# Kernel tuning notes

Measured on AMD Instinct MI355X. Metric: run time of the kernel, lower is better.

The kernel has to match this reference:

```python
import jax, jax.numpy as jnp
import numpy as np

N_HEAD = 16
HEAD_DIM = 64
ROPE_BASE = 10000.0


def _rope(t):
    # t: [B, H, C, D]; rotate-half RoPE, offset 0
    B, H, C, D = t.shape
    inv_freq = 1.0 / (ROPE_BASE ** (jnp.arange(0, D, 2, dtype=jnp.float32) / D))  # [D/2]
    ang = jnp.arange(C, dtype=jnp.float32)[:, None] * inv_freq[None, :]           # [C, D/2]
    cos = jnp.concatenate([jnp.cos(ang), jnp.cos(ang)], axis=-1)                  # [C, D]
    sin = jnp.concatenate([jnp.sin(ang), jnp.sin(ang)], axis=-1)                  # [C, D]
    t1, t2 = jnp.split(t, 2, axis=-1)
    rot = jnp.concatenate([-t2, t1], axis=-1)
    return t * cos.astype(t.dtype) + rot * sin.astype(t.dtype)


def setup_inputs() -> dict:
    key = jax.random.key(0)
    ks = jax.random.split(key, 5)
    E = 1024
    B, C = 2, 2048
    s = 1.0 / np.sqrt(E)
    return {
        "x": jax.random.normal(ks[0], (B, C, E), dtype=jnp.float32),
        "Wq": jax.random.normal(ks[1], (E, E), dtype=jnp.float32) * s,
        "Wk": jax.random.normal(ks[2], (E, E), dtype=jnp.float32) * s,
        "Wv": jax.random.normal(ks[3], (E, E), dtype=jnp.float32) * s,
        "Wo": jax.random.normal(ks[4], (E, E), dtype=jnp.float32) * s,
    }


def reference(x, Wq, Wk, Wv, Wo):
    B, C, E = x.shape
    H, D = N_HEAD, HEAD_DIM
    # nn.Linear(bias=False): y = x @ W.T
    Q = (x @ Wq.T).reshape(B, C, H, D).transpose(0, 2, 1, 3)  # [B,H,C,D]
    K = (x @ Wk.T).reshape(B, C, H, D).transpose(0, 2, 1, 3)
    V = (x @ Wv.T).reshape(B, C, H, D).transpose(0, 2, 1, 3)
    Q = _rope(Q)
    K = _rope(K)
    scores = jnp.einsum("bhqd,bhkd->bhqk", Q, K) / jnp.sqrt(jnp.float32(D))
    causal = jnp.tril(jnp.ones((C, C), dtype=bool))
    scores = jnp.where(causal, scores, jnp.float32(-jnp.inf))
    weights = jax.nn.softmax(scores, axis=-1)
    hidden = jnp.einsum("bhqk,bhkd->bhqd", weights, V)
    hidden = hidden.transpose(0, 2, 1, 3).reshape(B, C, H * D)
    return hidden @ Wo.T
```

## Files before the change

### kernel.cpp

```cpp
#include <hip/hip_runtime.h>
#include <hip/hip_bf16.h>

typedef __attribute__((ext_vector_type(8))) short bf16x8;
typedef __attribute__((ext_vector_type(4))) float f32x4;
typedef unsigned short u16;
typedef unsigned int u32;


__device__ __forceinline__ u16 f2bf(float f) {
  __hip_bfloat16 h = __float2bfloat16(f);
  return *reinterpret_cast<u16*>(&h);
}

__device__ __forceinline__ void async16(const void* g, void* l) {
  __builtin_amdgcn_global_load_lds((const __attribute__((address_space(1))) u32*)g,
                                   (__attribute__((address_space(3))) u32*)l, 16, 0, 0);
}


__global__ void cast_bf16(const float4* __restrict__ src, ushort4* __restrict__ dst, int n4) {
  int stride = gridDim.x * blockDim.x;
  for (int i = blockIdx.x * blockDim.x + threadIdx.x; i < n4; i += stride) {
    float4 v = src[i];
    ushort4 o;
    o.x = f2bf(v.x); o.y = f2bf(v.y); o.z = f2bf(v.z); o.w = f2bf(v.w);
    dst[i] = o;
  }
}

__global__ void cast_w4(const float4* __restrict__ w0, const float4* __restrict__ w1,
                        const float4* __restrict__ w2, const float4* __restrict__ w3,
                        ushort4* __restrict__ o0, ushort4* __restrict__ o1,
                        ushort4* __restrict__ o2, ushort4* __restrict__ o3, int n4) {
  const float4* src = (blockIdx.y == 0) ? w0 : (blockIdx.y == 1) ? w1 : (blockIdx.y == 2) ? w2 : w3;
  ushort4* dst = (blockIdx.y == 0) ? o0 : (blockIdx.y == 1) ? o1 : (blockIdx.y == 2) ? o2 : o3;
  int stride = gridDim.x * blockDim.x;
  for (int i = blockIdx.x * blockDim.x + threadIdx.x; i < n4; i += stride) {
    float4 v = src[i];
    ushort4 o;
    o.x = f2bf(v.x); o.y = f2bf(v.y); o.z = f2bf(v.z); o.w = f2bf(v.w);
    dst[i] = o;
  }
}


__global__ void rope_table(float* __restrict__ tcos, float* __restrict__ tsin) {
  int idx = blockIdx.x * blockDim.x + threadIdx.x;
  if (idx >= 2048 * 32) return;
  int c = idx >> 5, j = idx & 31;
  float inv = powf(10000.f, -(float)j * (1.f / 32.f));
  float ang = (float)c * inv;
  tcos[idx] = cosf(ang);
  tsin[idx] = sinf(ang);
}


__launch_bounds__(256)
__global__ void qkv_gemm(const u16* __restrict__ xb, const u16* __restrict__ Wqb,
                         const u16* __restrict__ Wkb, const u16* __restrict__ Wvb,
                         const float* __restrict__ tcos, const float* __restrict__ tsin,
                         u16* __restrict__ Qr, u16* __restrict__ Kr, u16* __restrict__ Vt) {
  const int z = blockIdx.z;
  const u16* W = (z == 0) ? Wqb : (z == 1) ? Wkb : Wvb;
  u16* dst = (z == 0) ? Qr : (z == 1) ? Kr : Vt;
  const int m0 = blockIdx.y * 128, n0 = blockIdx.x * 128;
  const int tid = threadIdx.x, w = tid >> 6, lane = tid & 63, g = lane >> 4, cl = lane & 15;
  const int wr = w >> 1, wc = w & 1;
  __shared__ u16 As[128][32], Bs[128][32];
  f32x4 acc[4][4] = {};
  for (int k0 = 0; k0 < 1024; k0 += 32) {
#pragma unroll
    for (int ch = 0; ch < 2; ++ch) {
      int t = tid + ch * 256;
      int row = t >> 2, col = (t & 3) * 8;
      async16(&xb[(size_t)(m0 + row) * 1024 + k0 + col], &As[row][col]);
      async16(&W[(size_t)(n0 + row) * 1024 + k0 + col], &Bs[row][col]);
    }
    __syncthreads();
    bf16x8 af[4], bfr[4];
#pragma unroll
    for (int i = 0; i < 4; ++i) af[i] = *(const bf16x8*)&As[wr * 64 + i * 16 + cl][g * 8];
#pragma unroll
    for (int j = 0; j < 4; ++j) bfr[j] = *(const bf16x8*)&Bs[wc * 64 + j * 16 + cl][g * 8];
#pragma unroll
    for (int i = 0; i < 4; ++i)
#pragma unroll
      for (int j = 0; j < 4; ++j)
        acc[i][j] = __builtin_amdgcn_mfma_f32_16x16x32_bf16(af[i], bfr[j], acc[i][j], 0, 0, 0);
    __syncthreads();
  }
  if (z < 2) {
#pragma unroll
    for (int i = 0; i < 4; ++i) {
      int mbase = m0 + wr * 64 + i * 16 + g * 4;
#pragma unroll
      for (int r = 0; r < 4; ++r) {
        int mm = mbase + r;
        int b = mm >> 11, pos = mm & 2047;
#pragma unroll
        for (int j = 0; j < 2; ++j) {
          int n = n0 + wc * 64 + j * 16 + cl;
          int h = n >> 6, dlo = n & 63;
          float a = acc[i][j][r], b2 = acc[i][j + 2][r];
          float cv = tcos[pos * 32 + dlo], sv = tsin[pos * 32 + dlo];
          float o1 = a * cv - b2 * sv;
          float o2 = b2 * cv + a * sv;
          size_t base = ((size_t)(b * 16 + h) * 2048 + pos) * 64;
          dst[base + dlo] = f2bf(o1);
          dst[base + dlo + 32] = f2bf(o2);
        }
      }
    }
  } else {
#pragma unroll
    for (int i = 0; i < 4; ++i) {
      int mbase = m0 + wr * 64 + i * 16 + g * 4;
      int b = mbase >> 11, pos = mbase & 2047;
#pragma unroll
      for (int j = 0; j < 4; ++j) {
        int n = n0 + wc * 64 + j * 16 + cl;
        int h = n >> 6, d = n & 63;
        ushort4 v4;
        v4.x = f2bf(acc[i][j][0]);
        v4.y = f2bf(acc[i][j][1]);
        v4.z = f2bf(acc[i][j][2]);
        v4.w = f2bf(acc[i][j][3]);
        *(ushort4*)&dst[((size_t)(b * 16 + h) * 64 + d) * 2048 + pos] = v4;
      }
    }
  }
}


__launch_bounds__(64)
__global__ void attn_kernel(const u16* __restrict__ Qr, const u16* __restrict__ Kr,
                            const u16* __restrict__ Vt, u16* __restrict__ hid) {
  const int bid = blockIdx.x;
  const int xcd = bid & 7, jj = bid >> 3;
  const int bh = xcd * 4 + (jj >> 6);
  const int qt = 63 - (jj & 63);
  const int lane = threadIdx.x, g = lane >> 4, cl = lane & 15;
  const int b = bh >> 4, h = bh & 15;
  const int qbase = qt * 32;
  const u16* Qp = Qr + (size_t)bh * 2048 * 64;
  const u16* Kp = Kr + (size_t)bh * 2048 * 64;
  const u16* Vp = Vt + (size_t)bh * 2048 * 64;
  __shared__ u16 P_lds[32 * 64];

  bf16x8 aq[4];
#pragma unroll
  for (int qg = 0; qg < 2; ++qg)
#pragma unroll
    for (int ks = 0; ks < 2; ++ks)
      aq[qg * 2 + ks] = *(const bf16x8*)&Qp[(size_t)(qbase + qg * 16 + cl) * 64 + ks * 32 + g * 8];

  f32x4 ot[8] = {};
  float mrow[8], lrow[8];
#pragma unroll
  for (int r = 0; r < 8; ++r) { mrow[r] = -__builtin_inff(); lrow[r] = 0.f; }

  const int ktmax = qt >> 1;

  auto loadK = [&](bf16x8* dst, int kt_) {
#pragma unroll
    for (int n = 0; n < 4; ++n)
#pragma unroll
      for (int ks = 0; ks < 2; ++ks)
        dst[n * 2 + ks] = *(const bf16x8*)&Kp[(size_t)(kt_ * 64 + n * 16 + cl) * 64 + ks * 32 + g * 8];
  };
  auto loadV = [&](bf16x8* dst, int kt_) {
#pragma unroll
    for (int ks = 0; ks < 2; ++ks)
#pragma unroll
      for (int j = 0; j < 4; ++j)
        dst[ks * 4 + j] = *(const bf16x8*)&Vp[(size_t)(j * 16 + cl) * 2048 + kt_ * 64 + ks * 32 + g * 8];
  };

  auto tile = [&](const bf16x8* kf, const bf16x8* bv, int kt_, bool diag) {
    f32x4 s[8] = {};
#pragma unroll
    for (int qg = 0; qg < 2; ++qg)
#pragma unroll
      for (int n = 0; n < 4; ++n)
#pragma unroll
        for (int ks = 0; ks < 2; ++ks)
          s[qg * 4 + n] = __builtin_amdgcn_mfma_f32_16x16x32_bf16(aq[qg * 2 + ks], kf[n * 2 + ks],
                                                                  s[qg * 4 + n], 0, 0, 0);
    if (diag) {
#pragma unroll
      for (int qg = 0; qg < 2; ++qg)
#pragma unroll
        for (int n = 0; n < 4; ++n)
#pragma unroll
          for (int r = 0; r < 4; ++r) {
            int q = qbase + qg * 16 + g * 4 + r, k = kt_ * 64 + n * 16 + cl;
            s[qg * 4 + n][r] = (k <= q) ? s[qg * 4 + n][r] * 0.125f : -__builtin_inff();
          }
    } else {
#pragma unroll
      for (int i = 0; i < 8; ++i)
#pragma unroll
        for (int r = 0; r < 4; ++r) s[i][r] *= 0.125f;
    }
    bf16x8 ap[4];
#pragma unroll
    for (int qg = 0; qg < 2; ++qg) {
      float pmax[4], ef[4];
#pragma unroll
      for (int r = 0; r < 4; ++r) {
        float v = fmaxf(fmaxf(s[qg * 4 + 0][r], s[qg * 4 + 1][r]),
                        fmaxf(s[qg * 4 + 2][r], s[qg * 4 + 3][r]));
#pragma unroll
        for (int off = 1; off < 16; off <<= 1) v = fmaxf(v, __shfl_xor(v, off));
        pmax[r] = v;
      }
#pragma unroll
      for (int r = 0; r < 4; ++r) {
        float mnew = fmaxf(mrow[qg * 4 + r], pmax[r]);
        ef[r] = __expf(mrow[qg * 4 + r] - mnew);
        mrow[qg * 4 + r] = mnew;
      }
      float rs[4] = {0.f, 0.f, 0.f, 0.f};
#pragma unroll
      for (int n = 0; n < 4; ++n)
#pragma unroll
        for (int r = 0; r < 4; ++r) {
          float p = __expf(s[qg * 4 + n][r] - mrow[qg * 4 + r]);
          s[qg * 4 + n][r] = p;
          rs[r] += p;
          int row = qg * 16 + g * 4 + r;
          P_lds[(row * 64 + n * 16 + cl) ^ ((row & 7) << 3)] = f2bf(p);
        }
#pragma unroll
      for (int r = 0; r < 4; ++r) {
        float v = rs[r];
#pragma unroll
        for (int off = 1; off < 16; off <<= 1) v += __shfl_xor(v, off);
        lrow[qg * 4 + r] = lrow[qg * 4 + r] * ef[r] + v;
      }
      int src = ((cl >> 2) << 4) | cl;
      float t0 = __shfl(ef[0], src), t1 = __shfl(ef[1], src);
      float t2 = __shfl(ef[2], src), t3 = __shfl(ef[3], src);
      float eft = (cl & 2) ? ((cl & 1) ? t3 : t2) : ((cl & 1) ? t1 : t0);
#pragma unroll
      for (int j = 0; j < 4; ++j)
#pragma unroll
        for (int r = 0; r < 4; ++r) ot[qg * 4 + j][r] *= eft;
#pragma unroll
      for (int ks = 0; ks < 2; ++ks) {
        int rowr = qg * 16 + cl;
        ap[qg * 2 + ks] = *(const bf16x8*)&P_lds[(rowr * 64 + ks * 32 + g * 8) ^ ((rowr & 7) << 3)];
      }
    }
#pragma unroll
    for (int qg = 0; qg < 2; ++qg)
#pragma unroll
      for (int ks = 0; ks < 2; ++ks)
#pragma unroll
        for (int j = 0; j < 4; ++j)
          ot[qg * 4 + j] = __builtin_amdgcn_mfma_f32_16x16x32_bf16(bv[ks * 4 + j], ap[qg * 2 + ks],
                                                                   ot[qg * 4 + j], 0, 0, 0);
  };

  bf16x8 kA[8], kB[8], bv[8];
  loadK(kA, 0);
  for (int kt = 0; kt <= ktmax; kt += 2) {
    loadV(bv, kt);
    if (kt + 1 <= ktmax) loadK(kB, kt + 1);
    tile(kA, bv, kt, kt == ktmax);
    if (kt + 1 <= ktmax) {
      loadV(bv, kt + 1);
      if (kt + 2 <= ktmax) loadK(kA, kt + 2);
      tile(kB, bv, kt + 1, kt + 1 == ktmax);
    }
  }

#pragma unroll
  for (int qg = 0; qg < 2; ++qg) {
    int src = ((cl >> 2) << 4) | cl;
    float t0 = __shfl(lrow[qg * 4 + 0], src), t1 = __shfl(lrow[qg * 4 + 1], src);
    float t2 = __shfl(lrow[qg * 4 + 2], src), t3 = __shfl(lrow[qg * 4 + 3], src);
    float lt = (cl & 2) ? ((cl & 1) ? t3 : t2) : ((cl & 1) ? t1 : t0);
    float inv = 1.f / lt;
    int q = qbase + qg * 16 + cl;
#pragma unroll
    for (int j = 0; j < 4; ++j) {
      ushort4 v4;
      v4.x = f2bf(ot[qg * 4 + j][0] * inv);
      v4.y = f2bf(ot[qg * 4 + j][1] * inv);
      v4.z = f2bf(ot[qg * 4 + j][2] * inv);
      v4.w = f2bf(ot[qg * 4 + j][3] * inv);
      *(ushort4*)&hid[((size_t)(b * 2048) + q) * 1024 + h * 64 + j * 16 + g * 4] = v4;
    }
  }
}


__launch_bounds__(256)
__global__ void out_gemm(const u16* __restrict__ hb, const u16* __restrict__ Wob,
                         float* __restrict__ out) {
  const int m0 = blockIdx.y * 128, n0 = blockIdx.x * 128;
  const int tid = threadIdx.x, w = tid >> 6, lane = tid & 63, g = lane >> 4, cl = lane & 15;
  const int wr = w >> 1, wc = w & 1;
  __shared__ u16 As[128][32], Bs[128][32];
  f32x4 acc[4][4] = {};
  for (int k0 = 0; k0 < 1024; k0 += 32) {
#pragma unroll
    for (int ch = 0; ch < 2; ++ch) {
      int t = tid + ch * 256;
      int row = t >> 2, col = (t & 3) * 8;
      async16(&hb[(size_t)(m0 + row) * 1024 + k0 + col], &As[row][col]);
      async16(&Wob[(size_t)(n0 + row) * 1024 + k0 + col], &Bs[row][col]);
    }
    __syncthreads();
    bf16x8 af[4], bfr[4];
#pragma unroll
    for (int i = 0; i < 4; ++i) af[i] = *(const bf16x8*)&As[wr * 64 + i * 16 + cl][g * 8];
#pragma unroll
    for (int j = 0; j < 4; ++j) bfr[j] = *(const bf16x8*)&Bs[wc * 64 + j * 16 + cl][g * 8];
#pragma unroll
    for (int i = 0; i < 4; ++i)
#pragma unroll
      for (int j = 0; j < 4; ++j)
        acc[i][j] = __builtin_amdgcn_mfma_f32_16x16x32_bf16(af[i], bfr[j], acc[i][j], 0, 0, 0);
    __syncthreads();
  }
#pragma unroll
  for (int i = 0; i < 4; ++i)
#pragma unroll
    for (int r = 0; r < 4; ++r) {
      int m = m0 + wr * 64 + i * 16 + g * 4 + r;
#pragma unroll
      for (int j = 0; j < 4; ++j)
        out[(size_t)m * 1024 + n0 + wc * 64 + j * 16 + cl] = acc[i][j][r];
    }
}


extern "C" void kernel_launch(void* const* d_in, const int* in_sizes, int n_in,
                              void* d_out, int out_size, void* d_ws, size_t ws_size,
                              hipStream_t stream) {
  const float* x = (const float*)d_in[0];
  const float* Wq = (const float*)d_in[1];
  const float* Wk = (const float*)d_in[2];
  const float* Wv = (const float*)d_in[3];
  const float* Wo = (const float*)d_in[4];
  float* out = (float*)d_out;

  char* ws = (char*)d_ws;
  size_t off = 0;
  auto alloc = [&](size_t bytes) {
    void* p = ws + off;
    off += (bytes + 255) & ~(size_t)255;
    return p;
  };
  u16* xb = (u16*)alloc(4096ull * 1024 * 2);
  u16* Wqb = (u16*)alloc(1024ull * 1024 * 2);
  u16* Wkb = (u16*)alloc(1024ull * 1024 * 2);
  u16* Wvb = (u16*)alloc(1024ull * 1024 * 2);
  u16* Wob = (u16*)alloc(1024ull * 1024 * 2);
  u16* Qr = (u16*)alloc(4096ull * 1024 * 2);
  u16* Kr = (u16*)alloc(4096ull * 1024 * 2);
  u16* Vt = (u16*)alloc(4096ull * 1024 * 2);
  u16* hid = (u16*)alloc(4096ull * 1024 * 2);
  float* tcos = (float*)alloc(2048ull * 32 * 4);
  float* tsin = (float*)alloc(2048ull * 32 * 4);

  cast_bf16<<<1024, 256, 0, stream>>>((const float4*)x, (ushort4*)xb, 4096 * 1024 / 4);
  cast_w4<<<dim3(256, 4), 256, 0, stream>>>((const float4*)Wq, (const float4*)Wk,
                                            (const float4*)Wv, (const float4*)Wo,
                                            (ushort4*)Wqb, (ushort4*)Wkb,
                                            (ushort4*)Wvb, (ushort4*)Wob, 1024 * 1024 / 4);
  rope_table<<<256, 256, 0, stream>>>(tcos, tsin);

  qkv_gemm<<<dim3(8, 32, 3), 256, 0, stream>>>(xb, Wqb, Wkb, Wvb, tcos, tsin, Qr, Kr, Vt);
  attn_kernel<<<2048, 64, 0, stream>>>(Qr, Kr, Vt, hid);
  out_gemm<<<dim3(8, 32), 256, 0, stream>>>(hid, Wob, out);
}
```

Before: 275.7 us.

## Compute transposed scores in attention, use exp2 softmax and balanced tile order

The QK^T MFMA now takes K and Q as swapped operands, so each lane holds one query row across four key values. Row max and sum reductions then need only two cross-lane shuffles instead of four per row, and the per-row rescale factor no longer has to be redistributed between lanes. The softmax scale is folded with log2(e) so exp2f replaces __expf, and P is written to LDS as packed ushort4 stores. Block-to-query-tile mapping now pairs long and short causal tiles within each XCD group to balance work, which changes which tiles run concurrently.

Result: faster. 243.9 us (-11.5%).

```diff
diff --git a/kernel.cpp b/kernel.cpp
--- a/kernel.cpp
+++ b/kernel.cpp
@@ -5,6 +5,8 @@
 typedef __attribute__((ext_vector_type(4))) float f32x4;
 typedef unsigned short u16;
 typedef unsigned int u32;
+
+#define SM_SCALE 0.18033688f
 
 
 __device__ __forceinline__ u16 f2bf(float f) {
@@ -136,16 +138,16 @@
 __global__ void attn_kernel(const u16* __restrict__ Qr, const u16* __restrict__ Kr,
                             const u16* __restrict__ Vt, u16* __restrict__ hid) {
   const int bid = blockIdx.x;
-  const int xcd = bid & 7, jj = bid >> 3;
-  const int bh = xcd * 4 + (jj >> 6);
-  const int qt = 63 - (jj & 63);
+  const int xcd = bid & 7, c = (bid >> 3) & 31, slot = bid >> 8;
+  const int bh = xcd * 4 + (slot >> 1);
+  const int qt = (slot & 1) ? c : 63 - c;
   const int lane = threadIdx.x, g = lane >> 4, cl = lane & 15;
   const int b = bh >> 4, h = bh & 15;
   const int qbase = qt * 32;
   const u16* Qp = Qr + (size_t)bh * 2048 * 64;
   const u16* Kp = Kr + (size_t)bh * 2048 * 64;
   const u16* Vp = Vt + (size_t)bh * 2048 * 64;
-  __shared__ u16 P_lds[32 * 64];
+  __shared__ u16 Pt[32 * 64];
 
   bf16x8 aq[4];
 #pragma unroll
@@ -155,9 +157,9 @@
       aq[qg * 2 + ks] = *(const bf16x8*)&Qp[(size_t)(qbase + qg * 16 + cl) * 64 + ks * 32 + g * 8];
 
   f32x4 ot[8] = {};
-  float mrow[8], lrow[8];
-#pragma unroll
-  for (int r = 0; r < 8; ++r) { mrow[r] = -__builtin_inff(); lrow[r] = 0.f; }
+  float mrow[2], lrow[2];
+  mrow[0] = mrow[1] = -__builtin_inff();
+  lrow[0] = lrow[1] = 0.f;
 
   const int ktmax = qt >> 1;
 
@@ -177,80 +179,73 @@
   };
 
   auto tile = [&](const bf16x8* kf, const bf16x8* bv, int kt_, bool diag) {
-    f32x4 s[8] = {};
+    f32x4 st[8] = {};
 #pragma unroll
     for (int qg = 0; qg < 2; ++qg)
 #pragma unroll
       for (int n = 0; n < 4; ++n)
 #pragma unroll
         for (int ks = 0; ks < 2; ++ks)
-          s[qg * 4 + n] = __builtin_amdgcn_mfma_f32_16x16x32_bf16(aq[qg * 2 + ks], kf[n * 2 + ks],
-                                                                  s[qg * 4 + n], 0, 0, 0);
+          st[qg * 4 + n] = __builtin_amdgcn_mfma_f32_16x16x32_bf16(kf[n * 2 + ks], aq[qg * 2 + ks],
+                                                                   st[qg * 4 + n], 0, 0, 0);
     if (diag) {
 #pragma unroll
-      for (int qg = 0; qg < 2; ++qg)
+      for (int qg = 0; qg < 2; ++qg) {
+        int q = qbase + qg * 16 + cl;
 #pragma unroll
         for (int n = 0; n < 4; ++n)
 #pragma unroll
           for (int r = 0; r < 4; ++r) {
-            int q = qbase + qg * 16 + g * 4 + r, k = kt_ * 64 + n * 16 + cl;
-            s[qg * 4 + n][r] = (k <= q) ? s[qg * 4 + n][r] * 0.125f : -__builtin_inff();
+            int k = kt_ * 64 + n * 16 + g * 4 + r;
+            st[qg * 4 + n][r] = (k <= q) ? st[qg * 4 + n][r] * SM_SCALE : -__builtin_inff();
           }
+      }
     } else {
 #pragma unroll
       for (int i = 0; i < 8; ++i)
 #pragma unroll
-        for (int r = 0; r < 4; ++r) s[i][r] *= 0.125f;
+        for (int r = 0; r < 4; ++r) st[i][r] *= SM_SCALE;
     }
     bf16x8 ap[4];
 #pragma unroll
     for (int qg = 0; qg < 2; ++qg) {
-      float pmax[4], ef[4];
-#pragma unroll
-      for (int r = 0; r < 4; ++r) {
-        float v = fmaxf(fmaxf(s[qg * 4 + 0][r], s[qg * 4 + 1][r]),
-                        fmaxf(s[qg * 4 + 2][r], s[qg * 4 + 3][r]));
-#pragma unroll
-        for (int off = 1; off < 16; off <<= 1) v = fmaxf(v, __shfl_xor(v, off));
-        pmax[r] = v;
+      float v0 = fmaxf(fmaxf(st[qg * 4 + 0][0], st[qg * 4 + 0][1]),
+                       fmaxf(st[qg * 4 + 0][2], st[qg * 4 + 0][3]));
+      float v1 = fmaxf(fmaxf(st[qg * 4 + 1][0], st[qg * 4 + 1][1]),
+                       fmaxf(st[qg * 4 + 1][2], st[qg * 4 + 1][3]));
+      float v2 = fmaxf(fmaxf(st[qg * 4 + 2][0], st[qg * 4 + 2][1]),
+                       fmaxf(st[qg * 4 + 2][2], st[qg * 4 + 2][3]));
+      float v3 = fmaxf(fmaxf(st[qg * 4 + 3][0], st[qg * 4 + 3][1]),
+                       fmaxf(st[qg * 4 + 3][2], st[qg * 4 + 3][3]));
+      float v = fmaxf(fmaxf(v0, v1), fmaxf(v2, v3));
+      v = fmaxf(v, __shfl_xor(v, 16));
+      v = fmaxf(v, __shfl_xor(v, 32));
+      float mnew = fmaxf(mrow[qg], v);
+      float ef = exp2f(mrow[qg] - mnew);
+      mrow[qg] = mnew;
+      float rs = 0.f;
+      int rowq = qg * 16 + cl;
+#pragma unroll
+      for (int n = 0; n < 4; ++n) {
+        float p0 = exp2f(st[qg * 4 + n][0] - mnew);
+        float p1 = exp2f(st[qg * 4 + n][1] - mnew);
+        float p2 = exp2f(st[qg * 4 + n][2] - mnew);
+        float p3 = exp2f(st[qg * 4 + n][3] - mnew);
+        rs += (p0 + p1) + (p2 + p3);
+        ushort4 v4;
+        v4.x = f2bf(p0); v4.y = f2bf(p1); v4.z = f2bf(p2); v4.w = f2bf(p3);
+        *(ushort4*)&Pt[(rowq * 64 + n * 16 + g * 4) ^ ((rowq & 7) << 3)] = v4;
       }
-#pragma unroll
-      for (int r = 0; r < 4; ++r) {
-        float mnew = fmaxf(mrow[qg * 4 + r], pmax[r]);
-        ef[r] = __expf(mrow[qg * 4 + r] - mnew);
-        mrow[qg * 4 + r] = mnew;
-      }
-      float rs[4] = {0.f, 0.f, 0.f, 0.f};
-#pragma unroll
-      for (int n = 0; n < 4; ++n)
-#pragma unroll
-        for (int r = 0; r < 4; ++r) {
-          float p = __expf(s[qg * 4 + n][r] - mrow[qg * 4 + r]);
-          s[qg * 4 + n][r] = p;
-          rs[r] += p;
-          int row = qg * 16 + g * 4 + r;
-          P_lds[(row * 64 + n * 16 + cl) ^ ((row & 7) << 3)] = f2bf(p);
-        }
-#pragma unroll
-      for (int r = 0; r < 4; ++r) {
-        float v = rs[r];
-#pragma unroll
-        for (int off = 1; off < 16; off <<= 1) v += __shfl_xor(v, off);
-        lrow[qg * 4 + r] = lrow[qg * 4 + r] * ef[r] + v;
-      }
-      int src = ((cl >> 2) << 4) | cl;
-      float t0 = __shfl(ef[0], src), t1 = __shfl(ef[1], src);
-      float t2 = __shfl(ef[2], src), t3 = __shfl(ef[3], src);
-      float eft = (cl & 2) ? ((cl & 1) ? t3 : t2) : ((cl & 1) ? t1 : t0);
-#pragma unroll
-      for (int j = 0; j < 4; ++j)
-#pragma unroll
-        for (int r = 0; r < 4; ++r) ot[qg * 4 + j][r] *= eft;
-#pragma unroll
-      for (int ks = 0; ks < 2; ++ks) {
-        int rowr = qg * 16 + cl;
-        ap[qg * 2 + ks] = *(const bf16x8*)&P_lds[(rowr * 64 + ks * 32 + g * 8) ^ ((rowr & 7) << 3)];
-      }
+      rs += __shfl_xor(rs, 16);
+      rs += __shfl_xor(rs, 32);
+      lrow[qg] = lrow[qg] * ef + rs;
+#pragma unroll
+      for (int j = 0; j < 4; ++j)
+#pragma unroll
+        for (int r = 0; r < 4; ++r) ot[qg * 4 + j][r] *= ef;
+#pragma unroll
+      for (int ks = 0; ks < 2; ++ks)
+        ap[qg * 2 + ks] = *(const bf16x8*)&Pt[(rowq * 64 + ks * 32 + g * 8) ^ ((rowq & 7) << 3)];
     }
 #pragma unroll
     for (int qg = 0; qg < 2; ++qg)
@@ -277,11 +272,7 @@
 
 #pragma unroll
   for (int qg = 0; qg < 2; ++qg) {
-    int src = ((cl >> 2) << 4) | cl;
-    float t0 = __shfl(lrow[qg * 4 + 0], src), t1 = __shfl(lrow[qg * 4 + 1], src);
-    float t2 = __shfl(lrow[qg * 4 + 2], src), t3 = __shfl(lrow[qg * 4 + 3], src);
-    float lt = (cl & 2) ? ((cl & 1) ? t3 : t2) : ((cl & 1) ? t1 : t0);
-    float inv = 1.f / lt;
+    float inv = 1.f / lrow[qg];
     int q = qbase + qg * 16 + cl;
 #pragma unroll
     for (int j = 0; j < 4; ++j) {
```
